# Optimization experiments

Hardware: AMD Instinct MI355X
Metric: run time of the kernel (lower is better)

Reference implementation:

```python
import jax, jax.numpy as jnp
import numpy as np

B, H, W, C = 16, 56, 56, 512
P = 7           # partition (window) size
NH, DH = 16, 32 # n_heads, head_dim (NH*DH == C)
EPS = 1e-6      # flax nnx LayerNorm default epsilon

def _rel_index(size):
    coords = np.stack(np.meshgrid(np.arange(size), np.arange(size), indexing='ij')).reshape(2, -1)
    rel = coords[:, :, None] - coords[:, None, :]
    rh = rel[0] + (size - 1)
    rw = rel[1] + (size - 1)
    return jnp.asarray(rh * (2 * size - 1) + rw)  # [P*P, P*P] int

REL_IDX = _rel_index(P)

def setup_inputs() -> dict:
    key = jax.random.key(0)
    ks = jax.random.split(key, 6)
    s = lambda k, shape: jax.random.normal(k, shape, jnp.float32) * 0.02
    return {
        'x': jax.random.normal(ks[0], (B, H, W, C), jnp.float32),
        'ln1_s': jnp.ones((C,), jnp.float32), 'ln1_b': jnp.zeros((C,), jnp.float32),
        'w_qkv': s(ks[1], (C, 3 * C)), 'b_qkv': jnp.zeros((3 * C,), jnp.float32),
        'bias_table': s(ks[2], ((2 * P - 1) ** 2, NH)),
        'w_merge': s(ks[3], (C, C)), 'b_merge': jnp.zeros((C,), jnp.float32),
        'ln2_s': jnp.ones((C,), jnp.float32), 'ln2_b': jnp.zeros((C,), jnp.float32),
        'w1': s(ks[4], (C, 4 * C)), 'b1': jnp.zeros((4 * C,), jnp.float32),
        'w2': s(ks[5], (4 * C, C)), 'b2': jnp.zeros((C,), jnp.float32),
    }

def _ln(x, s, b):
    m = x.mean(-1, keepdims=True)
    v = ((x - m) ** 2).mean(-1, keepdims=True)
    return (x - m) * jax.lax.rsqrt(v + EPS) * s + b

def reference(x, ln1_s, ln1_b, w_qkv, b_qkv, bias_table, w_merge, b_merge,
              ln2_s, ln2_b, w1, b1, w2, b2):
    Bn, Hh, Ww, Cc = x.shape
    HP, WP = Hh // P, Ww // P
    # window partition: [B,H,W,C] -> [B, G=HP*WP, P*P, C]
    xp = x.reshape(Bn, HP, P, WP, P, Cc).transpose(0, 1, 3, 2, 4, 5).reshape(Bn, HP * WP, P * P, Cc)
    # --- attention block (pre-LN) ---
    h = _ln(xp, ln1_s, ln1_b)
    qkv = h @ w_qkv + b_qkv
    q, k, v = jnp.split(qkv, 3, axis=-1)
    heads = lambda t: t.reshape(Bn, HP * WP, P * P, NH, DH).transpose(0, 1, 3, 2, 4)
    q = heads(q)
    k = heads(k) * (Cc ** -0.5)  # module scales by feat_dim**-0.5 (faithful)
    v = heads(v)
    # relative position bias gather: [NH, P*P, P*P]
    bias = bias_table[REL_IDX.reshape(-1)].reshape(P * P, P * P, NH).transpose(2, 0, 1)
    scores = jnp.einsum('bghid,bghjd->bghij', q, k) + bias
    attn = jax.nn.softmax(scores, axis=-1)
    o = jnp.einsum('bghij,bghjd->bghid', attn, v)
    o = o.transpose(0, 1, 3, 2, 4).reshape(Bn, HP * WP, P * P, Cc)
    xp = xp + (o @ w_merge + b_merge)
    # --- MLP block (pre-LN) ---
    m = _ln(xp, ln2_s, ln2_b)
    xp = xp + (jax.nn.gelu(m @ w1 + b1) @ w2 + b2)
    # window departition: [B, G, P*P, C] -> [B, H, W, C]
    return xp.reshape(Bn, HP, WP, P, P, Cc).transpose(0, 1, 3, 2, 4, 5).reshape(Bn, Hh, Ww, Cc)
```

## Files before the change

kernel.cpp:

```cpp
#include <hip/hip_runtime.h>
#include <stdint.h>

typedef unsigned short u16;
typedef u16    u16x8  __attribute__((ext_vector_type(8)));
typedef __bf16 bf16x8 __attribute__((ext_vector_type(8)));
typedef float  f32x4  __attribute__((ext_vector_type(4)));

#define TOKS 50176
#define CD   512

__device__ __forceinline__ float bf2f(u16 u) {
    union { unsigned int i; float f; } c; c.i = ((unsigned int)u) << 16; return c.f;
}
__device__ __forceinline__ u16 f2bf(float f) {
    union { float f; unsigned int i; } c; c.f = f;
    unsigned int x = c.i;
    return (u16)((x + 0x7fffu + ((x >> 16) & 1u)) >> 16);
}
__device__ __forceinline__ float gelu_tanh(float x) {
    float t = 0.7978845608028654f * (x + 0.044715f * x * x * x);
    float e = __expf(2.0f * t);
    float th = 1.0f - 2.0f / (e + 1.0f);
    return 0.5f * x * (1.0f + th);
}

typedef const __attribute__((address_space(1))) unsigned int gas_u32;
typedef __attribute__((address_space(3))) unsigned int las_u32;
__device__ __forceinline__ void gload16(const u16* g, u16* l) {
    __builtin_amdgcn_global_load_lds((gas_u32*)g, (las_u32*)l, 16, 0, 0);
}

__global__ __launch_bounds__(256)
void k_transpose_cast(const float* __restrict__ src, u16* __restrict__ dst,
                      const int K, const int N)
{
    __shared__ float tile[32][33];
    const int tx = threadIdx.x & 31, ty = threadIdx.x >> 5;
    const int n0 = blockIdx.x * 32, k0 = blockIdx.y * 32;
    #pragma unroll
    for (int i = 0; i < 4; ++i) {
        int r = ty + i * 8;
        tile[r][tx] = src[(size_t)(k0 + r) * N + n0 + tx];
    }
    __syncthreads();
    #pragma unroll
    for (int i = 0; i < 4; ++i) {
        int r = ty + i * 8;
        dst[(size_t)(n0 + r) * K + k0 + tx] = f2bf(tile[tx][r]);
    }
}

template<int BF>
__global__ __launch_bounds__(256)
void k_layernorm(const void* __restrict__ xin, const float* __restrict__ g,
                 const float* __restrict__ bvec, u16* __restrict__ out)
{
    const int l = threadIdx.x & 63;
    const int w = threadIdx.x >> 6;
    const size_t row = (size_t)blockIdx.x * 4 + w;
    const int c = l * 8;
    float v[8];
    if (BF) {
        u16x8 u = *(const u16x8*)((const u16*)xin + row * CD + c);
        #pragma unroll
        for (int i = 0; i < 8; ++i) v[i] = bf2f(u[i]);
    } else {
        f32x4 a0 = *(const f32x4*)((const float*)xin + row * CD + c);
        f32x4 a1 = *(const f32x4*)((const float*)xin + row * CD + c + 4);
        #pragma unroll
        for (int i = 0; i < 4; ++i) { v[i] = a0[i]; v[4 + i] = a1[i]; }
    }
    float s = 0.f, sq = 0.f;
    #pragma unroll
    for (int i = 0; i < 8; ++i) { s += v[i]; sq += v[i] * v[i]; }
    #pragma unroll
    for (int off = 32; off > 0; off >>= 1) {
        s  += __shfl_xor(s, off);
        sq += __shfl_xor(sq, off);
    }
    const float mean = s * (1.0f / 512.0f);
    const float var  = fmaxf(sq * (1.0f / 512.0f) - mean * mean, 0.0f);
    const float rstd = rsqrtf(var + 1e-6f);
    f32x4 g0 = *(const f32x4*)(g + c),    g1 = *(const f32x4*)(g + c + 4);
    f32x4 b0 = *(const f32x4*)(bvec + c), b1 = *(const f32x4*)(bvec + c + 4);
    u16x8 o;
    #pragma unroll
    for (int i = 0; i < 4; ++i) o[i]     = f2bf((v[i] - mean) * rstd * g0[i] + b0[i]);
    #pragma unroll
    for (int i = 0; i < 4; ++i) o[4 + i] = f2bf((v[4+i] - mean) * rstd * g1[i] + b1[i]);
    *(u16x8*)(out + row * CD + c) = o;
}

template<int EPI>
__global__ __launch_bounds__(512, 2)
void k_gemm256(const u16* __restrict__ A, const u16* __restrict__ Bt,
               const float* __restrict__ bias,
               const float* __restrict__ residf, const u16* __restrict__ residb,
               u16* __restrict__ outb, float* __restrict__ outf,
               const int N, const int K)
{
    __shared__ u16 As[2][8192];
    __shared__ u16 Bs[2][8192];
    const int t  = threadIdx.x;
    const int l  = t & 63;
    const int w  = t >> 6;
    const int wr = w >> 2, wc = w & 3;
    const int m0 = blockIdx.y * 256, n0 = blockIdx.x * 256;
    const int kq = l >> 4, fr = l & 15;

    int srow0, scol0, srow1, scol1;
    {
        int r0 = t >> 2, s0 = t & 3;
        srow0 = r0; scol0 = (s0 ^ ((r0 >> 1) & 3)) * 8;
        int sl = 512 + t;
        int r1 = sl >> 2, s1 = sl & 3;
        srow1 = r1; scol1 = (s1 ^ ((r1 >> 1) & 3)) * 8;
    }
    const u16* Asrc0 = A  + (size_t)(m0 + srow0) * K + scol0;
    const u16* Asrc1 = A  + (size_t)(m0 + srow1) * K + scol1;
    const u16* Bsrc0 = Bt + (size_t)(n0 + srow0) * K + scol0;
    const u16* Bsrc1 = Bt + (size_t)(n0 + srow1) * K + scol1;
    const int dst0 = w * 512;
    const int dst1 = 4096 + w * 512;

    int offA[8], offB[4];
    #pragma unroll
    for (int mi = 0; mi < 8; ++mi) {
        int r = wr * 128 + mi * 16 + fr;
        offA[mi] = r * 32 + (kq ^ ((r >> 1) & 3)) * 8;
    }
    #pragma unroll
    for (int ni = 0; ni < 4; ++ni) {
        int r = wc * 64 + ni * 16 + fr;
        offB[ni] = r * 32 + (kq ^ ((r >> 1) & 3)) * 8;
    }

    f32x4 acc[8][4];
    #pragma unroll
    for (int i = 0; i < 8; ++i)
        #pragma unroll
        for (int j = 0; j < 4; ++j) {
            f32x4 z = {0.f, 0.f, 0.f, 0.f};
            acc[i][j] = z;
        }

    const int nt = K >> 5;
    gload16(Asrc0, &As[0][dst0]); gload16(Asrc1, &As[0][dst1]);
    gload16(Bsrc0, &Bs[0][dst0]); gload16(Bsrc1, &Bs[0][dst1]);
    asm volatile("s_waitcnt vmcnt(0)" ::: "memory");
    __syncthreads();

    for (int tt = 0; tt < nt; ++tt) {
        const int cur = tt & 1;
        if (tt + 1 < nt) {
            const int nxt = cur ^ 1;
            const int ko  = (tt + 1) << 5;
            gload16(Asrc0 + ko, &As[nxt][dst0]); gload16(Asrc1 + ko, &As[nxt][dst1]);
            gload16(Bsrc0 + ko, &Bs[nxt][dst0]); gload16(Bsrc1 + ko, &Bs[nxt][dst1]);
        }
        bf16x8 af[8], bfv[4];
        #pragma unroll
        for (int mi = 0; mi < 8; ++mi) af[mi]  = *(const bf16x8*)&As[cur][offA[mi]];
        #pragma unroll
        for (int ni = 0; ni < 4; ++ni) bfv[ni] = *(const bf16x8*)&Bs[cur][offB[ni]];
        __builtin_amdgcn_s_setprio(1);
        #pragma unroll
        for (int mi = 0; mi < 8; ++mi)
            #pragma unroll
            for (int ni = 0; ni < 4; ++ni)
                acc[mi][ni] = __builtin_amdgcn_mfma_f32_16x16x32_bf16(
                    af[mi], bfv[ni], acc[mi][ni], 0, 0, 0);
        __builtin_amdgcn_s_setprio(0);
        asm volatile("s_waitcnt vmcnt(0)" ::: "memory");
        __syncthreads();
    }

    float bv[4];
    #pragma unroll
    for (int ni = 0; ni < 4; ++ni) bv[ni] = bias[n0 + wc * 64 + ni * 16 + fr];

    #pragma unroll
    for (int mi = 0; mi < 8; ++mi) {
        #pragma unroll
        for (int r = 0; r < 4; ++r) {
            const size_t row  = (size_t)(m0 + wr * 128 + mi * 16 + kq * 4 + r);
            const size_t base = row * N + n0 + wc * 64 + fr;
            #pragma unroll
            for (int ni = 0; ni < 4; ++ni) {
                float v = acc[mi][ni][r] + bv[ni];
                if (EPI == 1) v = gelu_tanh(v);
                if (EPI == 2) v += residf[base + ni * 16];
                if (EPI == 3) { v += bf2f(residb[base + ni * 16]); outf[base + ni * 16] = v; }
                else outb[base + ni * 16] = f2bf(v);
            }
        }
    }
}

__global__ __launch_bounds__(64)
void k_attn(const u16* __restrict__ qkv, const float* __restrict__ btab,
            u16* __restrict__ o, const int tok_base)
{
    __shared__ float Ss[64 * 53];
    const int l    = threadIdx.x;
    const int widl = blockIdx.x >> 4;
    const int head = blockIdx.x & 15;
    const int bl   = widl >> 6;
    const int g    = widl & 63;
    const int gh   = g >> 3, gw = g & 7;
    const int tok00 = bl * 3136 + gh * 392 + gw * 7;
    const int pl = (l < 49) ? l : 48;
    const int ph = pl / 7, pw = pl - (pl / 7) * 7;
    const int tokl = tok00 + ph * 56 + pw;

    float q[32];
    {
        const size_t qoff = (size_t)tokl * 1536 + head * 32;
        #pragma unroll
        for (int i = 0; i < 4; ++i) {
            u16x8 u = *(const u16x8*)(qkv + qoff + i * 8);
            #pragma unroll
            for (int j = 0; j < 8; ++j) q[i * 8 + j] = bf2f(u[j]);
        }
    }

    float rowmax = -1e30f;
    {
        int j = 0;
        for (int jh = 0; jh < 7; ++jh) {
            for (int jw = 0; jw < 7; ++jw, ++j) {
                const size_t koff = (size_t)(tok00 + jh * 56 + jw) * 1536 + 512 + head * 32;
                float d0 = 0.f, d1 = 0.f, d2 = 0.f, d3 = 0.f;
                #pragma unroll
                for (int i = 0; i < 4; ++i) {
                    u16x8 u = *(const u16x8*)(qkv + koff + i * 8);
                    d0 += q[i * 8 + 0] * bf2f(u[0]); d0 += q[i * 8 + 1] * bf2f(u[1]);
                    d1 += q[i * 8 + 2] * bf2f(u[2]); d1 += q[i * 8 + 3] * bf2f(u[3]);
                    d2 += q[i * 8 + 4] * bf2f(u[4]); d2 += q[i * 8 + 5] * bf2f(u[5]);
                    d3 += q[i * 8 + 6] * bf2f(u[6]); d3 += q[i * 8 + 7] * bf2f(u[7]);
                }
                const float bias = btab[(size_t)((ph - jh + 6) * 13 + (pw - jw + 6)) * 16 + head];
                const float sc = (d0 + d1 + d2 + d3) * 0.04419417382415922f + bias;
                rowmax = fmaxf(rowmax, sc);
                Ss[l * 53 + j] = sc;
            }
        }
    }

    float sum = 0.f;
    for (int j = 0; j < 49; ++j) {
        float p = __expf(Ss[l * 53 + j] - rowmax);
        sum += p;
        Ss[l * 53 + j] = p;
    }

    float oa[32];
    #pragma unroll
    for (int i = 0; i < 32; ++i) oa[i] = 0.f;
    {
        int j = 0;
        for (int jh = 0; jh < 7; ++jh) {
            for (int jw = 0; jw < 7; ++jw, ++j) {
                const size_t voff = (size_t)(tok00 + jh * 56 + jw) * 1536 + 1024 + head * 32;
                const float p = Ss[l * 53 + j];
                #pragma unroll
                for (int i = 0; i < 4; ++i) {
                    u16x8 u = *(const u16x8*)(qkv + voff + i * 8);
                    #pragma unroll
                    for (int jj = 0; jj < 8; ++jj) oa[i * 8 + jj] += p * bf2f(u[jj]);
                }
            }
        }
    }

    if (l < 49) {
        const float inv = 1.0f / sum;
        const size_t obase = (size_t)(tok_base + tokl) * CD + head * 32;
        #pragma unroll
        for (int i = 0; i < 4; ++i) {
            u16x8 u;
            #pragma unroll
            for (int jj = 0; jj < 8; ++jj) u[jj] = f2bf(oa[i * 8 + jj] * inv);
            *(u16x8*)(o + obase + i * 8) = u;
        }
    }
}

extern "C" void kernel_launch(void* const* d_in, const int* in_sizes, int n_in,
                              void* d_out, int out_size, void* d_ws, size_t ws_size,
                              hipStream_t stream)
{
    (void)in_sizes; (void)n_in; (void)out_size; (void)ws_size;
    const float* x     = (const float*)d_in[0];
    const float* ln1_s = (const float*)d_in[1];
    const float* ln1_b = (const float*)d_in[2];
    const float* w_qkv = (const float*)d_in[3];
    const float* b_qkv = (const float*)d_in[4];
    const float* btab  = (const float*)d_in[5];
    const float* w_mrg = (const float*)d_in[6];
    const float* b_mrg = (const float*)d_in[7];
    const float* ln2_s = (const float*)d_in[8];
    const float* ln2_b = (const float*)d_in[9];
    const float* w1    = (const float*)d_in[10];
    const float* b1    = (const float*)d_in[11];
    const float* w2    = (const float*)d_in[12];
    const float* b2    = (const float*)d_in[13];
    float* out = (float*)d_out;

    u16* wqkvT = (u16*)d_ws;
    u16* wmrgT = wqkvT + (size_t)1536 * 512;
    u16* w1T   = wmrgT + (size_t)512 * 512;
    u16* w2T   = w1T   + (size_t)2048 * 512;
    u16* hbuf  = w2T   + (size_t)512 * 2048;
    u16* mbuf  = hbuf  + (size_t)TOKS * 512;
    u16* y1    = mbuf  + (size_t)TOKS * 512;
    u16* qkvc  = y1    + (size_t)TOKS * 512;
    u16* hidc  = qkvc  + (size_t)12544 * 1536;

    dim3 B256(256), B512(512);

    k_transpose_cast<<<dim3(48, 16), B256, 0, stream>>>(w_qkv, wqkvT, 512, 1536);
    k_transpose_cast<<<dim3(16, 16), B256, 0, stream>>>(w_mrg, wmrgT, 512, 512);
    k_transpose_cast<<<dim3(64, 16), B256, 0, stream>>>(w1,   w1T,   512, 2048);
    k_transpose_cast<<<dim3(16, 64), B256, 0, stream>>>(w2,   w2T,   2048, 512);

    k_layernorm<0><<<dim3(TOKS / 4), B256, 0, stream>>>(x, ln1_s, ln1_b, hbuf);

    for (int c = 0; c < 4; ++c) {
        const size_t tb = (size_t)c * 12544;
        k_gemm256<0><<<dim3(6, 49), B512, 0, stream>>>(
            hbuf + tb * 512, wqkvT, b_qkv, nullptr, nullptr, qkvc, nullptr, 1536, 512);
        k_attn<<<dim3(256 * 16), dim3(64), 0, stream>>>(qkvc, btab, hbuf, (int)tb);
    }

    k_gemm256<2><<<dim3(2, 196), B512, 0, stream>>>(
        hbuf, wmrgT, b_mrg, x, nullptr, y1, nullptr, 512, 512);

    k_layernorm<1><<<dim3(TOKS / 4), B256, 0, stream>>>(y1, ln2_s, ln2_b, mbuf);

    for (int c = 0; c < 2; ++c) {
        const size_t rb = (size_t)c * 25088;
        k_gemm256<1><<<dim3(8, 98), B512, 0, stream>>>(
            mbuf + rb * 512, w1T, b1, nullptr, nullptr, hidc, nullptr, 2048, 512);
        k_gemm256<3><<<dim3(2, 98), B512, 0, stream>>>(
            hidc, w2T, b2, nullptr, y1 + rb * 512, nullptr, out + rb * 512, 512, 2048);
    }
}
```

Baseline: 1.242 ms.

## Triple-buffer GEMM LDS pipeline and remap workgroups per XCD

The 256x256 GEMM kernel moves from double to triple LDS buffering. It prefetches two K-tiles ahead and uses a single barrier per iteration, with a partial vmcnt wait, instead of a full drain plus syncthreads after every tile. The 2D grid is flattened to 1D, and workgroup IDs are remapped so each XCD gets a contiguous chunk of output tiles, which is meant to improve L2 reuse of A and B panels. The catch is that LDS per block grows to 96KB, so the launch bound of 2 blocks per CU may no longer fit and occupancy could fall.

```diff
diff --git a/kernel.cpp b/kernel.cpp
--- a/kernel.cpp
+++ b/kernel.cpp
@@ -97,42 +97,42 @@
                const float* __restrict__ bias,
                const float* __restrict__ residf, const u16* __restrict__ residb,
                u16* __restrict__ outb, float* __restrict__ outf,
-               const int N, const int K)
-{
-    __shared__ u16 As[2][8192];
-    __shared__ u16 Bs[2][8192];
+               const int N, const int K, const int nbx)
+{
+    __shared__ u16 As[3][8192];
+    __shared__ u16 Bs[3][8192];
     const int t  = threadIdx.x;
     const int l  = t & 63;
     const int w  = t >> 6;
     const int wr = w >> 2, wc = w & 3;
-    const int m0 = blockIdx.y * 256, n0 = blockIdx.x * 256;
+    const int nwg = gridDim.x;
+    const int q = nwg >> 3, r = nwg & 7;
+    const int xcd = blockIdx.x & 7, bix = blockIdx.x >> 3;
+    const int wg = (xcd < r ? xcd * (q + 1) : r * (q + 1) + (xcd - r) * q) + bix;
+    const int m0 = (wg / nbx) * 256, n0 = (wg % nbx) * 256;
     const int kq = l >> 4, fr = l & 15;
 
-    int srow0, scol0, srow1, scol1;
-    {
-        int r0 = t >> 2, s0 = t & 3;
-        srow0 = r0; scol0 = (s0 ^ ((r0 >> 1) & 3)) * 8;
-        int sl = 512 + t;
-        int r1 = sl >> 2, s1 = sl & 3;
-        srow1 = r1; scol1 = (s1 ^ ((r1 >> 1) & 3)) * 8;
-    }
-    const u16* Asrc0 = A  + (size_t)(m0 + srow0) * K + scol0;
-    const u16* Asrc1 = A  + (size_t)(m0 + srow1) * K + scol1;
-    const u16* Bsrc0 = Bt + (size_t)(n0 + srow0) * K + scol0;
-    const u16* Bsrc1 = Bt + (size_t)(n0 + srow1) * K + scol1;
+    const int row0 = t >> 2, q0 = t & 3;
+    const int col0 = (q0 ^ ((row0 >> 1) & 3)) * 8;
+    const int row1 = 128 + row0;
+    const int col1 = (q0 ^ ((row1 >> 1) & 3)) * 8;
+    const u16* Asrc0 = A  + (size_t)(m0 + row0) * K + col0;
+    const u16* Asrc1 = A  + (size_t)(m0 + row1) * K + col1;
+    const u16* Bsrc0 = Bt + (size_t)(n0 + row0) * K + col0;
+    const u16* Bsrc1 = Bt + (size_t)(n0 + row1) * K + col1;
     const int dst0 = w * 512;
     const int dst1 = 4096 + w * 512;
 
     int offA[8], offB[4];
     #pragma unroll
     for (int mi = 0; mi < 8; ++mi) {
-        int r = wr * 128 + mi * 16 + fr;
-        offA[mi] = r * 32 + (kq ^ ((r >> 1) & 3)) * 8;
+        int rr = wr * 128 + mi * 16 + fr;
+        offA[mi] = rr * 32 + (kq ^ ((rr >> 1) & 3)) * 8;
     }
     #pragma unroll
     for (int ni = 0; ni < 4; ++ni) {
-        int r = wc * 64 + ni * 16 + fr;
-        offB[ni] = r * 32 + (kq ^ ((r >> 1) & 3)) * 8;
+        int rr = wc * 64 + ni * 16 + fr;
+        offB[ni] = rr * 32 + (kq ^ ((rr >> 1) & 3)) * 8;
     }
 
     f32x4 acc[8][4];
@@ -145,18 +145,24 @@
         }
 
     const int nt = K >> 5;
-    gload16(Asrc0, &As[0][dst0]); gload16(Asrc1, &As[0][dst1]);
-    gload16(Bsrc0, &Bs[0][dst0]); gload16(Bsrc1, &Bs[0][dst1]);
-    asm volatile("s_waitcnt vmcnt(0)" ::: "memory");
-    __syncthreads();
-
+    {
+        gload16(Asrc0,      &As[0][dst0]); gload16(Asrc1,      &As[0][dst1]);
+        gload16(Bsrc0,      &Bs[0][dst0]); gload16(Bsrc1,      &Bs[0][dst1]);
+        gload16(Asrc0 + 32, &As[1][dst0]); gload16(Asrc1 + 32, &As[1][dst1]);
+        gload16(Bsrc0 + 32, &Bs[1][dst0]); gload16(Bsrc1 + 32, &Bs[1][dst1]);
+    }
+
+    int cur = 0;
     for (int tt = 0; tt < nt; ++tt) {
-        const int cur = tt & 1;
-        if (tt + 1 < nt) {
-            const int nxt = cur ^ 1;
-            const int ko  = (tt + 1) << 5;
-            gload16(Asrc0 + ko, &As[nxt][dst0]); gload16(Asrc1 + ko, &As[nxt][dst1]);
-            gload16(Bsrc0 + ko, &Bs[nxt][dst0]); gload16(Bsrc1 + ko, &Bs[nxt][dst1]);
+        if (tt == nt - 1) { asm volatile("s_waitcnt vmcnt(0)" ::: "memory"); }
+        else              { asm volatile("s_waitcnt vmcnt(4)" ::: "memory"); }
+        __builtin_amdgcn_s_barrier();
+        __builtin_amdgcn_sched_barrier(0);
+        if (tt + 2 < nt) {
+            const int pb = (cur == 0) ? 2 : cur - 1;
+            const int ko = (tt + 2) << 5;
+            gload16(Asrc0 + ko, &As[pb][dst0]); gload16(Asrc1 + ko, &As[pb][dst1]);
+            gload16(Bsrc0 + ko, &Bs[pb][dst0]); gload16(Bsrc1 + ko, &Bs[pb][dst1]);
         }
         bf16x8 af[8], bfv[4];
         #pragma unroll
@@ -171,8 +177,7 @@
                 acc[mi][ni] = __builtin_amdgcn_mfma_f32_16x16x32_bf16(
                     af[mi], bfv[ni], acc[mi][ni], 0, 0, 0);
         __builtin_amdgcn_s_setprio(0);
-        asm volatile("s_waitcnt vmcnt(0)" ::: "memory");
-        __syncthreads();
+        cur = (cur == 2) ? 0 : cur + 1;
     }
 
     float bv[4];
@@ -182,12 +187,12 @@
     #pragma unroll
     for (int mi = 0; mi < 8; ++mi) {
         #pragma unroll
-        for (int r = 0; r < 4; ++r) {
-            const size_t row  = (size_t)(m0 + wr * 128 + mi * 16 + kq * 4 + r);
+        for (int rr = 0; rr < 4; ++rr) {
+            const size_t row  = (size_t)(m0 + wr * 128 + mi * 16 + kq * 4 + rr);
             const size_t base = row * N + n0 + wc * 64 + fr;
             #pragma unroll
             for (int ni = 0; ni < 4; ++ni) {
-                float v = acc[mi][ni][r] + bv[ni];
+                float v = acc[mi][ni][rr] + bv[ni];
                 if (EPI == 1) v = gelu_tanh(v);
                 if (EPI == 2) v += residf[base + ni * 16];
                 if (EPI == 3) { v += bf2f(residb[base + ni * 16]); outf[base + ni * 16] = v; }
@@ -328,21 +333,21 @@
 
     for (int c = 0; c < 4; ++c) {
         const size_t tb = (size_t)c * 12544;
-        k_gemm256<0><<<dim3(6, 49), B512, 0, stream>>>(
-            hbuf + tb * 512, wqkvT, b_qkv, nullptr, nullptr, qkvc, nullptr, 1536, 512);
+        k_gemm256<0><<<dim3(49 * 6), B512, 0, stream>>>(
+            hbuf + tb * 512, wqkvT, b_qkv, nullptr, nullptr, qkvc, nullptr, 1536, 512, 6);
         k_attn<<<dim3(256 * 16), dim3(64), 0, stream>>>(qkvc, btab, hbuf, (int)tb);
     }
 
-    k_gemm256<2><<<dim3(2, 196), B512, 0, stream>>>(
-        hbuf, wmrgT, b_mrg, x, nullptr, y1, nullptr, 512, 512);
+    k_gemm256<2><<<dim3(196 * 2), B512, 0, stream>>>(
+        hbuf, wmrgT, b_mrg, x, nullptr, y1, nullptr, 512, 512, 2);
 
     k_layernorm<1><<<dim3(TOKS / 4), B256, 0, stream>>>(y1, ln2_s, ln2_b, mbuf);
 
     for (int c = 0; c < 2; ++c) {
         const size_t rb = (size_t)c * 25088;
-        k_gemm256<1><<<dim3(8, 98), B512, 0, stream>>>(
-            mbuf + rb * 512, w1T, b1, nullptr, nullptr, hidc, nullptr, 2048, 512);
-        k_gemm256<3><<<dim3(2, 98), B512, 0, stream>>>(
-            hidc, w2T, b2, nullptr, y1 + rb * 512, nullptr, out + rb * 512, 512, 2048);
-    }
-}
+        k_gemm256<1><<<dim3(98 * 8), B512, 0, stream>>>(
+            mbuf + rb * 512, w1T, b1, nullptr, nullptr, hidc, nullptr, 2048, 512, 8);
+        k_gemm256<3><<<dim3(98 * 2), B512, 0, stream>>>(
+            hidc, w2T, b2, nullptr, y1 + rb * 512, nullptr, out + rb * 512, 512, 2048, 2);
+    }
+}
```

Measured after the change: 1.222 ms. Within noise of the previous version (-1.6%).
